# Optimization experiments

Hardware: AMD Instinct MI355X
Metric: run time of the kernel (lower is better)

Reference implementation:

```python
import jax, jax.numpy as jnp
import numpy as np

N = 2048   # number of proposals
D = 128    # appearance feature dim
DK = 64    # key/query dim
DG = 64    # geometric embedding dim
SD = 8     # single relation output dim = appear_dim / N_r = 128/16


def setup_inputs() -> dict:
    key = jax.random.key(0)
    ks = jax.random.split(key, 10)
    s = jnp.float32(0.05)
    return {
        "appearance_feature": jax.random.normal(ks[0], (N, D), jnp.float32),
        "geometric_feature": jax.random.uniform(ks[1], (N, N, DG), jnp.float32),
        "Wv": jax.random.normal(ks[2], (D, SD), jnp.float32) * s,
        "bv": jnp.zeros((SD,), jnp.float32),
        "Wk": jax.random.normal(ks[3], (D, DK), jnp.float32) * s,
        "bk": jnp.zeros((DK,), jnp.float32),
        "Wq": jax.random.normal(ks[4], (D, DK), jnp.float32) * s,
        "bq": jnp.zeros((DK,), jnp.float32),
        "Wg": jax.random.normal(ks[5], (DG, 1), jnp.float32) * s,
        "bg": jnp.zeros((1,), jnp.float32),
    }


def reference(appearance_feature, geometric_feature, Wv, bv, Wk, bk, Wq, bq, Wg, bg):
    n = geometric_feature.shape[0]
    # value projection: [N, SD]
    appear = appearance_feature @ Wv + bv
    # key/query projections: [N, DK]
    k = appearance_feature @ Wk + bk
    q = appearance_feature @ Wq + bq
    # appearance attention logits: [N, N]
    w_A = (k @ q.T) * (1.0 / jnp.sqrt(jnp.float32(DK)))
    # geometric gate: relu(W_G(geom)) -> [N, N]
    w_G = jax.nn.relu(
        (geometric_feature.reshape(-1, DG) @ Wg + bg).reshape(n, n)
    )
    # gated exp, normalized over axis 0 (as in the source: torch.sum(w_nominator, 0))
    w_nom = w_G * jnp.exp(w_A)
    w = w_nom / jnp.sum(w_nom, axis=0, keepdims=True)
    # weighted sum of values: [N, SD]
    return w @ appear
```

## Files before the change

### kernel.cpp

```cpp
#include <hip/hip_runtime.h>

#define N 2048
#define D 128
#define DK 64
#define DG 64
#define SD 8
#define TI 16
#define TJ 256

__global__ __launch_bounds__(128) void proj_kernel(
    const float* __restrict__ A,
    const float* __restrict__ Wv, const float* __restrict__ bv,
    const float* __restrict__ Wk, const float* __restrict__ bk,
    const float* __restrict__ Wq, const float* __restrict__ bq,
    float* __restrict__ kout, float* __restrict__ qout, float* __restrict__ vout)
{
    __shared__ float arow[D];
    const int i = blockIdx.x;
    const int t = threadIdx.x;
    arow[t] = A[(size_t)i * D + t];
    __syncthreads();
    for (int e = t; e < 2 * DK + SD; e += 128) {
        const float* W; const float* b; int od; int col;
        if (e < DK)            { W = Wk; b = bk; od = DK; col = e; }
        else if (e < 2 * DK)   { W = Wq; b = bq; od = DK; col = e - DK; }
        else                   { W = Wv; b = bv; od = SD; col = e - 2 * DK; }
        float acc = 0.f;
        #pragma unroll 8
        for (int c = 0; c < D; ++c) acc += arow[c] * W[c * od + col];
        acc += b[col];
        if (e < DK)          kout[(size_t)i * DK + col] = acc;
        else if (e < 2 * DK) qout[(size_t)i * DK + col] = acc;
        else                 vout[(size_t)i * SD + col] = acc;
    }
}

__global__ __launch_bounds__(256) void gate_kernel(
    const float* __restrict__ geom,
    const float* __restrict__ Wg, const float* __restrict__ bg,
    const float* __restrict__ kin, const float* __restrict__ qin,
    float* __restrict__ w_nom, float* __restrict__ colpartial)
{
    __shared__ float wA[TI * TJ];
    __shared__ float kt[TI * DK];
    const int tid = threadIdx.x;
    const int j0 = blockIdx.x * TJ;
    const int i0 = blockIdx.y * TI;

    for (int e = tid; e < TI * DK; e += 256) kt[e] = kin[(size_t)i0 * DK + e];
    __syncthreads();

    {
        float acc[TI];
        #pragma unroll
        for (int r = 0; r < TI; ++r) acc[r] = 0.f;
        const float4* ktv = (const float4*)kt;
        const float4* qrow = (const float4*)(qin + (size_t)(j0 + tid) * DK);
        #pragma unroll
        for (int chunk = 0; chunk < 2; ++chunk) {
            float4 qv[8];
            #pragma unroll
            for (int m = 0; m < 8; ++m) qv[m] = qrow[chunk * 8 + m];
            #pragma unroll
            for (int r = 0; r < TI; ++r) {
                float p = 0.f;
                #pragma unroll
                for (int m = 0; m < 8; ++m) {
                    float4 kv = ktv[r * 16 + chunk * 8 + m];
                    p += kv.x * qv[m].x + kv.y * qv[m].y + kv.z * qv[m].z + kv.w * qv[m].w;
                }
                acc[r] += p;
            }
        }
        #pragma unroll
        for (int r = 0; r < TI; ++r) wA[r * TJ + tid] = expf(acc[r] * 0.125f);
    }
    __syncthreads();

    const int group = tid >> 4;
    const int sub = tid & 15;
    const float4 wg4 = ((const float4*)Wg)[sub];
    const float bgv = bg[0];

    float colacc[16];
    #pragma unroll
    for (int cc = 0; cc < 16; ++cc) colacc[cc] = 0.f;

    for (int ii = 0; ii < TI; ++ii) {
        const int row = i0 + ii;
        const float4* grow = (const float4*)(geom + ((size_t)row * N + j0) * DG);
        #pragma unroll
        for (int cc = 0; cc < 16; ++cc) {
            const int jl = cc * 16 + group;
            float4 g4 = grow[(size_t)jl * 16 + sub];
            float s = g4.x * wg4.x + g4.y * wg4.y + g4.z * wg4.z + g4.w * wg4.w;
            s += __shfl_xor(s, 1);
            s += __shfl_xor(s, 2);
            s += __shfl_xor(s, 4);
            s += __shfl_xor(s, 8);
            s += bgv;
            s = s > 0.f ? s : 0.f;
            float val = s * wA[ii * TJ + jl];
            colacc[cc] += val;
            if (sub == 0) w_nom[(size_t)row * N + j0 + jl] = val;
        }
    }
    if (sub == 0) {
        #pragma unroll
        for (int cc = 0; cc < 16; ++cc)
            colpartial[(size_t)blockIdx.y * N + j0 + cc * 16 + group] = colacc[cc];
    }
}

__global__ __launch_bounds__(256) void colsum_kernel(
    const float* __restrict__ colpartial, float* __restrict__ colsum)
{
    const int j = blockIdx.x * 256 + threadIdx.x;
    float acc = 0.f;
    #pragma unroll 8
    for (int r = 0; r < 128; ++r) acc += colpartial[(size_t)r * N + j];
    colsum[j] = acc;
}

__global__ __launch_bounds__(256) void out_kernel(
    const float* __restrict__ w_nom, const float* __restrict__ colsum,
    const float* __restrict__ appear, float* __restrict__ out)
{
    const int i = blockIdx.x;
    const int t = threadIdx.x;
    float acc[SD];
    #pragma unroll
    for (int s = 0; s < SD; ++s) acc[s] = 0.f;

    for (int j = t; j < N; j += 256) {
        float wn = w_nom[(size_t)i * N + j];
        float inv = wn / colsum[j];
        const float4* ap = (const float4*)(appear + (size_t)j * SD);
        float4 a0 = ap[0], a1 = ap[1];
        acc[0] += inv * a0.x; acc[1] += inv * a0.y;
        acc[2] += inv * a0.z; acc[3] += inv * a0.w;
        acc[4] += inv * a1.x; acc[5] += inv * a1.y;
        acc[6] += inv * a1.z; acc[7] += inv * a1.w;
    }
    #pragma unroll
    for (int s = 0; s < SD; ++s) {
        #pragma unroll
        for (int off = 32; off >= 1; off >>= 1)
            acc[s] += __shfl_down(acc[s], off);
    }
    __shared__ float red[4][SD];
    const int wave = t >> 6;
    const int lane = t & 63;
    if (lane == 0) {
        #pragma unroll
        for (int s = 0; s < SD; ++s) red[wave][s] = acc[s];
    }
    __syncthreads();
    if (t < SD) out[(size_t)i * SD + t] = red[0][t] + red[1][t] + red[2][t] + red[3][t];
}

extern "C" void kernel_launch(void* const* d_in, const int* in_sizes, int n_in,
                              void* d_out, int out_size, void* d_ws, size_t ws_size,
                              hipStream_t stream) {
    const float* A    = (const float*)d_in[0];
    const float* geom = (const float*)d_in[1];
    const float* Wv   = (const float*)d_in[2];
    const float* bv   = (const float*)d_in[3];
    const float* Wk   = (const float*)d_in[4];
    const float* bk   = (const float*)d_in[5];
    const float* Wq   = (const float*)d_in[6];
    const float* bq   = (const float*)d_in[7];
    const float* Wg   = (const float*)d_in[8];
    const float* bg   = (const float*)d_in[9];
    float* out = (float*)d_out;

    float* ws = (float*)d_ws;
    float* kbuf       = ws;
    float* qbuf       = kbuf + (size_t)N * DK;
    float* appear     = qbuf + (size_t)N * DK;
    float* w_nom      = appear + (size_t)N * SD;
    float* colpartial = w_nom + (size_t)N * N;
    float* colsum     = colpartial + (size_t)(N / TI) * N;

    proj_kernel<<<N, 128, 0, stream>>>(A, Wv, bv, Wk, bk, Wq, bq, kbuf, qbuf, appear);
    gate_kernel<<<dim3(N / TJ, N / TI), 256, 0, stream>>>(geom, Wg, bg, kbuf, qbuf,
                                                          w_nom, colpartial);
    colsum_kernel<<<N / 256, 256, 0, stream>>>(colpartial, colsum);
    out_kernel<<<N, 256, 0, stream>>>(w_nom, colsum, appear, out);
}
```

Measured before the change: 300.2 us.

## Batch nontemporal geometry loads, stage w_nom in LDS, vectorize output pass

In the gate kernel, the row tile is halved to TI=8 so the grid has more blocks. Each row's 16 geometry float4 loads are issued up front as nontemporal loads to expose more memory parallelism. Gated values are written back into shared memory and then stored to w_nom as coalesced float4 rows instead of scattered single-lane stores. The column-sum kernel now stores reciprocals, and the output kernel reads w_nom and those reciprocals as float4 with a multiply instead of a divide. The trade-off is doubled colpartial traffic, more registers for the batched loads, and an extra sync.

```diff
diff --git a/kernel.cpp b/kernel.cpp
--- a/kernel.cpp
+++ b/kernel.cpp
@@ -5,8 +5,10 @@
 #define DK 64
 #define DG 64
 #define SD 8
-#define TI 16
+#define TI 8
 #define TJ 256
+
+typedef float f4v __attribute__((ext_vector_type(4)));
 
 __global__ __launch_bounds__(128) void proj_kernel(
     const float* __restrict__ A,
@@ -54,23 +56,20 @@
         float acc[TI];
         #pragma unroll
         for (int r = 0; r < TI; ++r) acc[r] = 0.f;
-        const float4* ktv = (const float4*)kt;
-        const float4* qrow = (const float4*)(qin + (size_t)(j0 + tid) * DK);
-        #pragma unroll
-        for (int chunk = 0; chunk < 2; ++chunk) {
-            float4 qv[8];
+        const f4v* ktv = (const f4v*)kt;
+        const f4v* qrow = (const f4v*)(qin + (size_t)(j0 + tid) * DK);
+        f4v qv[16];
+        #pragma unroll
+        for (int m = 0; m < 16; ++m) qv[m] = qrow[m];
+        #pragma unroll
+        for (int r = 0; r < TI; ++r) {
+            float p = 0.f;
             #pragma unroll
-            for (int m = 0; m < 8; ++m) qv[m] = qrow[chunk * 8 + m];
-            #pragma unroll
-            for (int r = 0; r < TI; ++r) {
-                float p = 0.f;
-                #pragma unroll
-                for (int m = 0; m < 8; ++m) {
-                    float4 kv = ktv[r * 16 + chunk * 8 + m];
-                    p += kv.x * qv[m].x + kv.y * qv[m].y + kv.z * qv[m].z + kv.w * qv[m].w;
-                }
-                acc[r] += p;
+            for (int m = 0; m < 16; ++m) {
+                f4v kv = ktv[r * 16 + m];
+                p += kv.x * qv[m].x + kv.y * qv[m].y + kv.z * qv[m].z + kv.w * qv[m].w;
             }
+            acc[r] = p;
         }
         #pragma unroll
         for (int r = 0; r < TI; ++r) wA[r * TJ + tid] = expf(acc[r] * 0.125f);
@@ -79,7 +78,7 @@
 
     const int group = tid >> 4;
     const int sub = tid & 15;
-    const float4 wg4 = ((const float4*)Wg)[sub];
+    const f4v wg4 = ((const f4v*)Wg)[sub];
     const float bgv = bg[0];
 
     float colacc[16];
@@ -87,22 +86,24 @@
     for (int cc = 0; cc < 16; ++cc) colacc[cc] = 0.f;
 
     for (int ii = 0; ii < TI; ++ii) {
-        const int row = i0 + ii;
-        const float4* grow = (const float4*)(geom + ((size_t)row * N + j0) * DG);
+        const f4v* grow = (const f4v*)(geom + ((size_t)(i0 + ii) * N + j0) * DG);
+        f4v g[16];
+        #pragma unroll
+        for (int cc = 0; cc < 16; ++cc)
+            g[cc] = __builtin_nontemporal_load(grow + (size_t)(cc * 16 + group) * 16 + sub);
         #pragma unroll
         for (int cc = 0; cc < 16; ++cc) {
-            const int jl = cc * 16 + group;
-            float4 g4 = grow[(size_t)jl * 16 + sub];
-            float s = g4.x * wg4.x + g4.y * wg4.y + g4.z * wg4.z + g4.w * wg4.w;
+            float s = g[cc].x * wg4.x + g[cc].y * wg4.y + g[cc].z * wg4.z + g[cc].w * wg4.w;
             s += __shfl_xor(s, 1);
             s += __shfl_xor(s, 2);
             s += __shfl_xor(s, 4);
             s += __shfl_xor(s, 8);
             s += bgv;
-            s = s > 0.f ? s : 0.f;
-            float val = s * wA[ii * TJ + jl];
+            s = fmaxf(s, 0.f);
+            const int jl = cc * 16 + group;
+            const float val = s * wA[ii * TJ + jl];
             colacc[cc] += val;
-            if (sub == 0) w_nom[(size_t)row * N + j0 + jl] = val;
+            if (sub == 0) wA[ii * TJ + jl] = val;
         }
     }
     if (sub == 0) {
@@ -110,20 +111,31 @@
         for (int cc = 0; cc < 16; ++cc)
             colpartial[(size_t)blockIdx.y * N + j0 + cc * 16 + group] = colacc[cc];
     }
+    __syncthreads();
+    {
+        const f4v* src = (const f4v*)wA;
+        #pragma unroll
+        for (int r = 0; r < TI * TJ / 4; r += 256) {
+            const int idx = r + tid;
+            const int row = idx >> 6;
+            const int col = idx & 63;
+            ((f4v*)(w_nom + (size_t)(i0 + row) * N + j0))[col] = src[idx];
+        }
+    }
 }
 
 __global__ __launch_bounds__(256) void colsum_kernel(
-    const float* __restrict__ colpartial, float* __restrict__ colsum)
+    const float* __restrict__ colpartial, float* __restrict__ colrcp)
 {
     const int j = blockIdx.x * 256 + threadIdx.x;
     float acc = 0.f;
     #pragma unroll 8
-    for (int r = 0; r < 128; ++r) acc += colpartial[(size_t)r * N + j];
-    colsum[j] = acc;
+    for (int r = 0; r < N / TI; ++r) acc += colpartial[(size_t)r * N + j];
+    colrcp[j] = 1.0f / acc;
 }
 
 __global__ __launch_bounds__(256) void out_kernel(
-    const float* __restrict__ w_nom, const float* __restrict__ colsum,
+    const float* __restrict__ w_nom, const float* __restrict__ colrcp,
     const float* __restrict__ appear, float* __restrict__ out)
 {
     const int i = blockIdx.x;
@@ -132,15 +144,26 @@
     #pragma unroll
     for (int s = 0; s < SD; ++s) acc[s] = 0.f;
 
-    for (int j = t; j < N; j += 256) {
-        float wn = w_nom[(size_t)i * N + j];
-        float inv = wn / colsum[j];
-        const float4* ap = (const float4*)(appear + (size_t)j * SD);
-        float4 a0 = ap[0], a1 = ap[1];
-        acc[0] += inv * a0.x; acc[1] += inv * a0.y;
-        acc[2] += inv * a0.z; acc[3] += inv * a0.w;
-        acc[4] += inv * a1.x; acc[5] += inv * a1.y;
-        acc[6] += inv * a1.z; acc[7] += inv * a1.w;
+    #pragma unroll
+    for (int jj = 0; jj < N / (256 * 4); ++jj) {
+        const int j4 = jj * 256 + t;
+        const f4v wn = ((const f4v*)(w_nom + (size_t)i * N))[j4];
+        const f4v rc = ((const f4v*)colrcp)[j4];
+        const float w0 = wn.x * rc.x, w1 = wn.y * rc.y, w2 = wn.z * rc.z, w3 = wn.w * rc.w;
+        const int j = j4 * 4;
+        const f4v* a0 = (const f4v*)(appear + (size_t)j * SD);
+        f4v r0 = a0[0], r1 = a0[1];
+        f4v r2 = a0[2], r3 = a0[3];
+        f4v r4 = a0[4], r5 = a0[5];
+        f4v r6 = a0[6], r7 = a0[7];
+        acc[0] += w0 * r0.x + w1 * r2.x + w2 * r4.x + w3 * r6.x;
+        acc[1] += w0 * r0.y + w1 * r2.y + w2 * r4.y + w3 * r6.y;
+        acc[2] += w0 * r0.z + w1 * r2.z + w2 * r4.z + w3 * r6.z;
+        acc[3] += w0 * r0.w + w1 * r2.w + w2 * r4.w + w3 * r6.w;
+        acc[4] += w0 * r1.x + w1 * r3.x + w2 * r5.x + w3 * r7.x;
+        acc[5] += w0 * r1.y + w1 * r3.y + w2 * r5.y + w3 * r7.y;
+        acc[6] += w0 * r1.z + w1 * r3.z + w2 * r5.z + w3 * r7.z;
+        acc[7] += w0 * r1.w + w1 * r3.w + w2 * r5.w + w3 * r7.w;
     }
     #pragma unroll
     for (int s = 0; s < SD; ++s) {
@@ -180,11 +203,11 @@
     float* appear     = qbuf + (size_t)N * DK;
     float* w_nom      = appear + (size_t)N * SD;
     float* colpartial = w_nom + (size_t)N * N;
-    float* colsum     = colpartial + (size_t)(N / TI) * N;
+    float* colrcp     = colpartial + (size_t)(N / TI) * N;
 
     proj_kernel<<<N, 128, 0, stream>>>(A, Wv, bv, Wk, bk, Wq, bq, kbuf, qbuf, appear);
     gate_kernel<<<dim3(N / TJ, N / TI), 256, 0, stream>>>(geom, Wg, bg, kbuf, qbuf,
                                                           w_nom, colpartial);
-    colsum_kernel<<<N / 256, 256, 0, stream>>>(colpartial, colsum);
-    out_kernel<<<N, 256, 0, stream>>>(w_nom, colsum, appear, out);
-}
+    colsum_kernel<<<N / 256, 256, 0, stream>>>(colpartial, colrcp);
+    out_kernel<<<N, 256, 0, stream>>>(w_nom, colrcp, appear, out);
+}
```

After: 243.7 us. 1.23x faster.
